# Optimization experiments

Measured on AMD Instinct MI355X. Metric: run time of the kernel, lower is better.

## Reference

```python
import jax, jax.numpy as jnp
import numpy as np

B, T, E, H, W = 2, 1024, 1024, 8, 31
D = 2 * W + 1  # head dim must equal 2*window_size+1 for the rel-pos broadcast


def _ln(x, w, b):
    mu = jnp.mean(x, axis=-1, keepdims=True)
    var = jnp.mean(jnp.square(x - mu), axis=-1, keepdims=True)
    return (x - mu) * jax.lax.rsqrt(var + 1e-5) * w + b


def setup_inputs() -> dict:
    key = jax.random.key(0)
    k = jax.random.split(key, 8)
    s = 0.02
    return {
        "x": jax.random.normal(k[0], (B, T, E // 2), jnp.float32),
        "ln1_w": jnp.ones(E, jnp.float32), "ln1_b": jnp.zeros(E, jnp.float32),
        "qkv_w": jax.random.normal(k[1], (3 * H * D, E), jnp.float32) * s,
        "qkv_b": jnp.zeros(3 * H * D, jnp.float32),
        "rel_pos": jax.random.normal(k[2], (D, D), jnp.float32) * s,
        "proj_w": jax.random.normal(k[3], (E, H * D), jnp.float32) * s,
        "proj_b": jnp.zeros(E, jnp.float32),
        "ln2_w": jnp.ones(E, jnp.float32), "ln2_b": jnp.zeros(E, jnp.float32),
        "fc_w": jax.random.normal(k[4], (4 * E, E), jnp.float32) * s,
        "fc_b": jnp.zeros(4 * E, jnp.float32),
        "cproj_w": jax.random.normal(k[5], (E, 4 * E), jnp.float32) * s,
        "cproj_b": jnp.zeros(E, jnp.float32),
    }


def reference(x, ln1_w, ln1_b, qkv_w, qkv_b, rel_pos, proj_w, proj_b,
              ln2_w, ln2_b, fc_w, fc_b, cproj_w, cproj_b):
    # --- RotaryEmbedding: angle = x * inv_freq; out = cat(sin, cos) -> [B,T,E]
    dim = 2 * x.shape[-1]
    inv_freq = 1.0 / 10000.0 ** (jnp.arange(0, dim, 2, dtype=jnp.float32) / dim)
    ang = x * inv_freq
    xr = jnp.concatenate([jnp.sin(ang), jnp.cos(ang)], axis=-1)  # [B,T,E]

    # --- custom windowed attention on ln_1(xr)
    h = _ln(xr, ln1_w, ln1_b)
    qkv = h @ qkv_w.T + qkv_b                       # [B,T,3*H*D]
    q, k, v = jnp.split(qkv, 3, axis=-1)

    def heads(t):
        return t.reshape(B, T, H, D).transpose(0, 2, 1, 3)  # [B,H,T,D]

    q, k, v = heads(q), heads(k), heads(v)
    # per-token q-outer-k scores (einsum '...bd,...bv->...bdv'): [B,H,T,D,D]
    scores = jnp.einsum('bhtd,bhtv->bhtdv', q, k)
    # rel-pos bias: Embedding lookup at offsets -W..W (negative indices wrap)
    bias = rel_pos[jnp.arange(-W, W + 1) % D]       # [D, D] == [2W+1, d_model]
    attn = jax.nn.softmax(scores + bias, axis=-2)   # softmax over non-canonical axis
    out = jnp.einsum('bhtdv,bhtv->bhtd', attn, v)   # apply per-token attn matrix to v
    out = out.transpose(0, 2, 1, 3).reshape(B, T, H * D)
    xa = xr + out @ proj_w.T + proj_b               # residual

    # --- MLP
    h2 = _ln(xa, ln2_w, ln2_b)
    m = jax.nn.gelu(h2 @ fc_w.T + fc_b, approximate=False) @ cproj_w.T + cproj_b
    return xa + m
```

## Files before the change

kernel.cpp:

```cpp
#include <hip/hip_runtime.h>
#include <hip/hip_bf16.h>


typedef __bf16 bf16;
typedef bf16 bf16x8 __attribute__((ext_vector_type(8)));
typedef bf16 bf16x4 __attribute__((ext_vector_type(4)));
typedef bf16 bf16x2 __attribute__((ext_vector_type(2)));
typedef float f32x4 __attribute__((ext_vector_type(4)));

__global__ __launch_bounds__(256) void rotary_ln_kernel(
    const float* __restrict__ x, const float* __restrict__ w,
    const float* __restrict__ b, float* __restrict__ xr, bf16* __restrict__ Y)
{
    const int row = blockIdx.x;
    const int tid = threadIdx.x;
    float2 xv = *(const float2*)(x + (size_t)row * 512 + tid * 2);
    float i0 = exp2f(-(float)(2*tid)     * 0.025952563241307518f);
    float i1 = exp2f(-(float)(2*tid + 1) * 0.025952563241307518f);
    float a0 = xv.x * i0, a1 = xv.y * i1;
    float s0 = sinf(a0), s1 = sinf(a1);
    float c0 = cosf(a0), c1 = cosf(a1);
    *(float2*)(xr + (size_t)row * 1024 + tid*2)       = make_float2(s0, s1);
    *(float2*)(xr + (size_t)row * 1024 + 512 + tid*2) = make_float2(c0, c1);
    float s  = s0 + s1 + c0 + c1;
    float ss = s0*s0 + s1*s1 + c0*c0 + c1*c1;
    #pragma unroll
    for (int off = 32; off > 0; off >>= 1) {
        s  += __shfl_down(s, off);
        ss += __shfl_down(ss, off);
    }
    __shared__ float rs[4], rss[4];
    int wave = tid >> 6, lane = tid & 63;
    if (lane == 0) { rs[wave] = s; rss[wave] = ss; }
    __syncthreads();
    s  = rs[0] + rs[1] + rs[2] + rs[3];
    ss = rss[0] + rss[1] + rss[2] + rss[3];
    float mu   = s * (1.f / 1024.f);
    float var  = ss * (1.f / 1024.f) - mu * mu;
    float rstd = rsqrtf(var + 1e-5f);
    float2 w0 = *(const float2*)(w + tid*2);
    float2 b0 = *(const float2*)(b + tid*2);
    float2 w1 = *(const float2*)(w + 512 + tid*2);
    float2 b1 = *(const float2*)(b + 512 + tid*2);
    bf16x2 y0, y1;
    y0[0] = (bf16)((s0 - mu) * rstd * w0.x + b0.x);
    y0[1] = (bf16)((s1 - mu) * rstd * w0.y + b0.y);
    y1[0] = (bf16)((c0 - mu) * rstd * w1.x + b1.x);
    y1[1] = (bf16)((c1 - mu) * rstd * w1.y + b1.y);
    *(bf16x2*)(Y + (size_t)row * 1024 + tid*2)       = y0;
    *(bf16x2*)(Y + (size_t)row * 1024 + 512 + tid*2) = y1;
}

__global__ __launch_bounds__(256) void ln_bf16_kernel(
    const float* __restrict__ X, const float* __restrict__ w,
    const float* __restrict__ b, bf16* __restrict__ Y)
{
    int row = blockIdx.x;
    const float4* xp = (const float4*)(X + (size_t)row * 1024);
    float4 xv = xp[threadIdx.x];
    float s  = xv.x + xv.y + xv.z + xv.w;
    float ss = xv.x*xv.x + xv.y*xv.y + xv.z*xv.z + xv.w*xv.w;
    #pragma unroll
    for (int off = 32; off > 0; off >>= 1) {
        s  += __shfl_down(s, off);
        ss += __shfl_down(ss, off);
    }
    __shared__ float rs[4], rss[4];
    int wave = threadIdx.x >> 6, lane = threadIdx.x & 63;
    if (lane == 0) { rs[wave] = s; rss[wave] = ss; }
    __syncthreads();
    s  = rs[0] + rs[1] + rs[2] + rs[3];
    ss = rss[0] + rss[1] + rss[2] + rss[3];
    float mu  = s * (1.f / 1024.f);
    float var = ss * (1.f / 1024.f) - mu * mu;
    float rstd = rsqrtf(var + 1e-5f);
    float4 wv = ((const float4*)w)[threadIdx.x];
    float4 bv = ((const float4*)b)[threadIdx.x];
    bf16 y[4];
    y[0] = (bf16)((xv.x - mu) * rstd * wv.x + bv.x);
    y[1] = (bf16)((xv.y - mu) * rstd * wv.y + bv.y);
    y[2] = (bf16)((xv.z - mu) * rstd * wv.z + bv.z);
    y[3] = (bf16)((xv.w - mu) * rstd * wv.w + bv.w);
    *(uint2*)(Y + (size_t)row * 1024 + threadIdx.x * 4) = *(uint2*)y;
}

__device__ __forceinline__ void conv_chunk(
    const float* __restrict__ src, bf16* __restrict__ dst,
    int ci, int N, int K, int Kp)
{
    int kpc = Kp >> 3;
    int r  = ci / kpc;
    int kc = (ci - r * kpc) << 3;
    bf16x8 o;
    if (r < N && kc < K) {
        float4 f0 = *(const float4*)(src + (size_t)r * K + kc);
        float4 f1 = *(const float4*)(src + (size_t)r * K + kc + 4);
        o[0]=(bf16)f0.x; o[1]=(bf16)f0.y; o[2]=(bf16)f0.z; o[3]=(bf16)f0.w;
        o[4]=(bf16)f1.x; o[5]=(bf16)f1.y; o[6]=(bf16)f1.z; o[7]=(bf16)f1.w;
    } else {
        #pragma unroll
        for (int j = 0; j < 8; ++j) o[j] = (bf16)0.f;
    }
    *(bf16x8*)(dst + (size_t)r * Kp + kc) = o;
}

__global__ __launch_bounds__(256) void conv_all_kernel(
    const float* __restrict__ qkv_w, const float* __restrict__ proj_w,
    const float* __restrict__ fc_w,  const float* __restrict__ cproj_w,
    const float* __restrict__ qkv_b,
    bf16* __restrict__ wqkv, bf16* __restrict__ wproj,
    bf16* __restrict__ wfc,  bf16* __restrict__ wcproj,
    float* __restrict__ qkvb_p)
{
    if (blockIdx.x == 5120) {
        for (int i = threadIdx.x; i < 1536; i += 256)
            qkvb_p[i] = (i < 1512) ? qkv_b[i] : 0.f;
        return;
    }
    int idx = blockIdx.x * 256 + threadIdx.x;
    if      (idx < 196608)  conv_chunk(qkv_w,   wqkv,   idx,          1512, 1024, 1024);
    else if (idx < 262144)  conv_chunk(proj_w,  wproj,  idx - 196608, 1024,  504,  512);
    else if (idx < 786432)  conv_chunk(fc_w,    wfc,    idx - 262144, 4096, 1024, 1024);
    else                    conv_chunk(cproj_w, wcproj, idx - 786432, 1024, 4096, 4096);
}

template<int N> __device__ __forceinline__ void vmwait()
{
    if constexpr      (N==0) asm volatile("s_waitcnt vmcnt(0)" ::: "memory");
    else if constexpr (N==4) asm volatile("s_waitcnt vmcnt(4)" ::: "memory");
    else if constexpr (N==6) asm volatile("s_waitcnt vmcnt(6)" ::: "memory");
}
__device__ __forceinline__ void lgkmwait0()
{
    asm volatile("s_waitcnt lgkmcnt(0)" ::: "memory");
}
__device__ __forceinline__ void hw_barrier()
{
    asm volatile("s_barrier" ::: "memory");
}

__device__ __forceinline__ void gload16(const char* src, char* ldsdst)
{
    __builtin_amdgcn_global_load_lds(
        (const __attribute__((address_space(1))) void*)src,
        (__attribute__((address_space(3))) void*)ldsdst, 16, 0, 0);
}

__device__ __forceinline__ float gelu_exact(float v)
{
    return 0.5f * v * (1.f + erff(v * 0.70710678118654752f));
}

template<int EPI>
__global__ __launch_bounds__(512, 2) void gemm8_kernel(
    const bf16* __restrict__ A, const bf16* __restrict__ Wt,
    const float* __restrict__ bias, bf16* __restrict__ Cb,
    int N, int Kp, int ksplit)
{
    __shared__ __align__(16) char lds[131072];

    const int tid  = threadIdx.x;
    const int w    = tid >> 6;
    const int lane = tid & 63;
    const int wm   = w >> 2;
    const int wn   = w & 3;
    const int rl   = lane & 15;
    const int lh   = lane >> 4;

    const int gx = gridDim.x, gy = gridDim.y;
    const int nwg = gx * gy * gridDim.z;
    const int chunk = nwg >> 3;
    int id = (blockIdx.z * gy + blockIdx.y) * gx + blockIdx.x;
    int sw = (id & 7) * chunk + (id >> 3);
    const int bx = sw % gx;
    const int t2 = sw / gx;
    const int by = t2 % gy;
    const int bz = t2 / gy;

    const int row0 = by * 128;
    const int col0 = bx * 256;
    const size_t strideBy = (size_t)Kp * 2;
    const size_t kz = (size_t)bz * ksplit * 2;
    const char* Abase = (const char*)A  + (size_t)row0 * strideBy + kz;
    const char* Wbase = (const char*)Wt + (size_t)col0 * strideBy + kz;

    size_t srcA[2], srcB[4];
    #pragma unroll
    for (int i = 0; i < 2; ++i) {
        int ls = i * 512 + tid;
        int r = ls >> 3, s = ls & 7;
        srcA[i] = (size_t)r * strideBy + (size_t)((s ^ (r & 7)) << 4);
    }
    #pragma unroll
    for (int i = 0; i < 4; ++i) {
        int ls = i * 512 + tid;
        int r = ls >> 3, s = ls & 7;
        srcB[i] = (size_t)r * strideBy + (size_t)((s ^ (r & 7)) << 4);
    }

    auto STAGE_A = [&](int buf, int kt) {
        const char* ab = Abase + (size_t)kt * 128;
        char* d = &lds[buf * 16384];
        #pragma unroll
        for (int i = 0; i < 2; ++i)
            gload16(ab + srcA[i], d + (i * 512 + tid) * 16);
    };
    auto STAGE_B = [&](int buf, int kt) {
        const char* wb = Wbase + (size_t)kt * 128;
        char* d = &lds[32768 + buf * 32768];
        #pragma unroll
        for (int i = 0; i < 4; ++i)
            gload16(wb + srcB[i], d + (i * 512 + tid) * 16);
    };

    f32x4 acc[4][4] = {};
    const int niter = ksplit >> 6;

    STAGE_A(0, 0);
    STAGE_B(0, 0);
    STAGE_B(1, 1);
    vmwait<4>();
    hw_barrier();

    int cb3 = 0, sb3 = 2;
    for (int kt = 0; kt < niter; ++kt) {
        if (kt + 1 < niter) STAGE_A((kt + 1) & 1, kt + 1);
        if (kt + 2 < niter) STAGE_B(sb3, kt + 2);

        const char* pA = &lds[(kt & 1) * 16384];
        const char* pB = &lds[32768 + cb3 * 32768];
        bf16x8 af[4][2], bq[4][2];
        #pragma unroll
        for (int mi = 0; mi < 4; ++mi) {
            int ar = wm * 64 + mi * 16 + rl;
            #pragma unroll
            for (int ks = 0; ks < 2; ++ks)
                af[mi][ks] = *(const bf16x8*)
                    (pA + ar * 128 + (((ks * 4 + lh) ^ (ar & 7)) << 4));
        }
        #pragma unroll
        for (int nj = 0; nj < 4; ++nj) {
            int br = wn * 64 + nj * 16 + rl;
            #pragma unroll
            for (int ks = 0; ks < 2; ++ks)
                bq[nj][ks] = *(const bf16x8*)
                    (pB + br * 128 + (((ks * 4 + lh) ^ (br & 7)) << 4));
        }
        __builtin_amdgcn_s_setprio(1);
        #pragma unroll
        for (int ks = 0; ks < 2; ++ks)
            #pragma unroll
            for (int mi = 0; mi < 4; ++mi)
                #pragma unroll
                for (int nj = 0; nj < 4; ++nj)
                    acc[mi][nj] = __builtin_amdgcn_mfma_f32_16x16x32_bf16(
                        af[mi][ks], bq[nj][ks], acc[mi][nj], 0, 0, 0);
        __builtin_amdgcn_s_setprio(0);

        if (kt + 1 < niter) {
            lgkmwait0();
            if (kt + 2 < niter) vmwait<4>();
            else                vmwait<0>();
            hw_barrier();
        }
        cb3 = (cb3 == 2) ? 0 : cb3 + 1;
        sb3 = (sb3 == 2) ? 0 : sb3 + 1;
    }

    const int rq = lh * 4;
    bf16* Cbz = Cb;
    if (EPI == 3) Cbz += (size_t)bz * 2048 * N;
    #pragma unroll
    for (int mi = 0; mi < 4; ++mi) {
        #pragma unroll
        for (int rj = 0; rj < 4; ++rj) {
            int row = row0 + wm * 64 + mi * 16 + rq + rj;
            #pragma unroll
            for (int nj = 0; nj < 4; ++nj) {
                int col = col0 + wn * 64 + nj * 16 + rl;
                float c = acc[mi][nj][rj];
                size_t off = (size_t)row * N + col;
                if (EPI == 1) Cbz[off] = (bf16)gelu_exact(c + bias[col]);
                else          Cbz[off] = (bf16)c;
            }
        }
    }
}

template<int EPI>
__global__ __launch_bounds__(256, 4) void gemm6_kernel(
    const bf16* __restrict__ A, const bf16* __restrict__ Wt,
    const float* __restrict__ bias,
    float* Cf, bf16* Cb, int N, int Kp, int ksplit)
{
    __shared__ __align__(16) char lds[2][12288];

    const int tid  = threadIdx.x;
    const int w    = tid >> 6;
    const int lane = tid & 63;

    const int gx = gridDim.x, gy = gridDim.y;
    const int nwg = gx * gy * gridDim.z;
    const int chunk = nwg >> 3;
    int id = (blockIdx.z * gy + blockIdx.y) * gx + blockIdx.x;
    int sw = (id & 7) * chunk + (id >> 3);
    const int bx = sw % gx;
    const int t2 = sw / gx;
    const int by = t2 % gy;
    const int bz = t2 / gy;

    const int row0 = by * 64;
    const int col0 = bx * 128;
    const int wr = (w >> 1) * 32;
    const int wc = (w & 1) * 64;
    const int rl = lane & 15;
    const int kb16 = (lane >> 4) * 16;

    const size_t strideBy = (size_t)Kp * 2;
    const size_t kz = (size_t)bz * ksplit * 2;
    const char* Abase = (const char*)A  + (size_t)row0 * strideBy + kz;
    const char* Wbase = (const char*)Wt + (size_t)col0 * strideBy + kz;

    const size_t srcA0 = (size_t)(tid >> 2) * strideBy + (tid & 3) * 16;
    size_t srcB[2];
    #pragma unroll
    for (int i = 0; i < 2; ++i) {
        int o = (i * 256 + tid) * 16;
        srcB[i] = (size_t)(o >> 6) * strideBy + (o & 63);
    }

    f32x4 acc[2][4] = {};

    auto STAGE = [&](int buf, int kt) {
        const char* ab = Abase + (size_t)kt * 64;
        const char* wb = Wbase + (size_t)kt * 64;
        gload16(ab + srcA0, &lds[buf][0] + tid * 16);
        #pragma unroll
        for (int i = 0; i < 2; ++i)
            gload16(wb + srcB[i], &lds[buf][4096] + (i * 256 + tid) * 16);
    };

    const int niter = ksplit >> 5;
    STAGE(0, 0);
    __syncthreads();
    for (int kt = 0; kt < niter; ++kt) {
        if (kt + 1 < niter)
            STAGE((kt + 1) & 1, kt + 1);
        const char* base = lds[kt & 1];
        bf16x8 af[2], bfr[4];
        #pragma unroll
        for (int mi = 0; mi < 2; ++mi)
            af[mi] = *(const bf16x8*)(base + ((wr + mi*16 + rl) << 6) + kb16);
        #pragma unroll
        for (int nj = 0; nj < 4; ++nj)
            bfr[nj] = *(const bf16x8*)(base + 4096 + ((wc + nj*16 + rl) << 6) + kb16);
        __builtin_amdgcn_s_setprio(1);
        #pragma unroll
        for (int mi = 0; mi < 2; ++mi)
            #pragma unroll
            for (int nj = 0; nj < 4; ++nj)
                acc[mi][nj] = __builtin_amdgcn_mfma_f32_16x16x32_bf16(
                    af[mi], bfr[nj], acc[mi][nj], 0, 0, 0);
        __builtin_amdgcn_s_setprio(0);
        __syncthreads();
    }

    const int rq = (lane >> 4) * 4;
    bf16* Cbz = Cb;
    if (EPI == 3) Cbz += (size_t)bz * 2048 * N;
    #pragma unroll
    for (int mi = 0; mi < 2; ++mi) {
        #pragma unroll
        for (int rj = 0; rj < 4; ++rj) {
            int row = row0 + wr + mi*16 + rq + rj;
            #pragma unroll
            for (int nj = 0; nj < 4; ++nj) {
                int col = col0 + wc + nj*16 + rl;
                float c = acc[mi][nj][rj];
                if (EPI != 3) c += bias[col];
                size_t off = (size_t)row * N + col;
                if (EPI == 0)      Cb[off]  = (bf16)c;
                else               Cbz[off] = (bf16)c;
            }
        }
    }
}

template<int P>
__global__ __launch_bounds__(256) void reduce_kernel(
    const bf16* __restrict__ parts, const float* __restrict__ bias,
    const float* R, float* out)
{
    int row = blockIdx.x;
    int c = threadIdx.x * 4;
    size_t off = (size_t)row * 1024 + c;
    float4 bv = *(const float4*)(bias + c);
    float4 o = *(const float4*)(R + off);
    o.x += bv.x; o.y += bv.y; o.z += bv.z; o.w += bv.w;
    #pragma unroll
    for (int p = 0; p < P; ++p) {
        bf16x4 v = *(const bf16x4*)(parts + (size_t)p * 2048 * 1024 + off);
        o.x += (float)v[0]; o.y += (float)v[1];
        o.z += (float)v[2]; o.w += (float)v[3];
    }
    *(float4*)(out + off) = o;
}

__global__ __launch_bounds__(256) void attn_kernel(
    const bf16* __restrict__ qkv, const float* __restrict__ rel_pos,
    bf16* __restrict__ outp)
{
    __shared__ float sbias[64*65];
    __shared__ float kmw[4][3][64];
    for (int i = threadIdx.x; i < 63*63; i += 256) {
        int d = i / 63, v = i - d*63;
        sbias[d*65 + v] = rel_pos[((d + 32) % 63) * 63 + v];
    }
    __syncthreads();
    const int wave = threadIdx.x >> 6;
    const int lane = threadIdx.x & 63;
    const int tk  = blockIdx.x * 4 + wave;
    const int row = tk >> 3;
    const int h   = tk & 7;
    const bf16* base = qkv + (size_t)row * 1536 + h * 63;
    float q_own = 0.f, k_own = 0.f, v_own = 0.f;
    if (lane < 63) {
        q_own = (float)base[lane];
        k_own = (float)base[504 + lane];
        v_own = (float)base[1008 + lane];
    }
    float m = -1e30f;
    for (int d = 0; d < 63; ++d) {
        float qd = __shfl(q_own, d);
        m = fmaxf(m, fmaf(qd, k_own, sbias[d*65 + lane]));
    }
    float Z = 0.f;
    for (int d = 0; d < 63; ++d) {
        float qd = __shfl(q_own, d);
        Z += __expf(fmaf(qd, k_own, sbias[d*65 + lane]) - m);
    }
    kmw[wave][0][lane] = k_own;
    kmw[wave][1][lane] = m;
    kmw[wave][2][lane] = v_own / Z;
    float acc = 0.f;
    for (int v = 0; v < 63; ++v) {
        float s = fmaf(q_own, kmw[wave][0][v], sbias[lane*65 + v]) - kmw[wave][1][v];
        acc += __expf(s) * kmw[wave][2][v];
    }
    if (lane < 63)
        outp[(size_t)row * 512 + h*63 + lane] = (bf16)acc;
    if (h == 7 && lane == 63) {
        #pragma unroll
        for (int j = 0; j < 8; ++j)
            outp[(size_t)row * 512 + 504 + j] = (bf16)0.f;
    }
}

extern "C" void kernel_launch(void* const* d_in, const int* in_sizes, int n_in,
                              void* d_out, int out_size, void* d_ws, size_t ws_size,
                              hipStream_t stream)
{
    const float* x       = (const float*)d_in[0];
    const float* ln1_w   = (const float*)d_in[1];
    const float* ln1_b   = (const float*)d_in[2];
    const float* qkv_w   = (const float*)d_in[3];
    const float* qkv_b   = (const float*)d_in[4];
    const float* rel_pos = (const float*)d_in[5];
    const float* proj_w  = (const float*)d_in[6];
    const float* proj_b  = (const float*)d_in[7];
    const float* ln2_w   = (const float*)d_in[8];
    const float* ln2_b   = (const float*)d_in[9];
    const float* fc_w    = (const float*)d_in[10];
    const float* fc_b    = (const float*)d_in[11];
    const float* cproj_w = (const float*)d_in[12];
    const float* cproj_b = (const float*)d_in[13];
    float* out = (float*)d_out;

    char* p = (char*)d_ws;
    float* xr      = (float*)p;            p += (size_t)2048*1024*4;
    bf16*  h_bf    = (bf16*)p;             p += (size_t)2048*1024*2;
    bf16*  wqkv    = (bf16*)p;             p += (size_t)1536*1024*2;
    bf16*  wproj   = (bf16*)p;             p += (size_t)1024*512*2;
    bf16*  wfc     = (bf16*)p;             p += (size_t)4096*1024*2;
    bf16*  wcproj  = (bf16*)p;             p += (size_t)1024*4096*2;
    float* qkvb_p  = (float*)p;            p += 8192;
    bf16*  attn_bf = (bf16*)p;             p += (size_t)2048*512*2;
    bf16*  qkvb    = (bf16*)p;
    bf16*  fc_act  = (bf16*)p;
    bf16*  proj_part = qkvb;
    bf16*  cp_part = (bf16*)d_ws;

    conv_all_kernel<<<5121, 256, 0, stream>>>(qkv_w, proj_w, fc_w, cproj_w, qkv_b,
                                              wqkv, wproj, wfc, wcproj, qkvb_p);
    rotary_ln_kernel<<<2048, 256, 0, stream>>>(x, ln1_w, ln1_b, xr, h_bf);
    gemm6_kernel<0><<<dim3(12,32,1), 256, 0, stream>>>(h_bf, wqkv, qkvb_p,
                                                       nullptr, qkvb, 1536, 1024, 1024);
    attn_kernel<<<4096, 256, 0, stream>>>(qkvb, rel_pos, attn_bf);
    gemm6_kernel<3><<<dim3(8,32,2), 256, 0, stream>>>(attn_bf, wproj, nullptr,
                                                      nullptr, proj_part, 1024, 512, 256);
    reduce_kernel<2><<<2048, 256, 0, stream>>>(proj_part, proj_b, xr, out);
    ln_bf16_kernel<<<2048, 256, 0, stream>>>(out, ln2_w, ln2_b, h_bf);
    gemm8_kernel<1><<<dim3(16,16,1), 512, 0, stream>>>(h_bf, wfc, fc_b,
                                                       fc_act, 4096, 1024, 1024);
    gemm8_kernel<3><<<dim3(4,16,4), 512, 0, stream>>>(fc_act, wcproj, nullptr,
                                                      cp_part, 1024, 4096, 1024);
    reduce_kernel<4><<<2048, 256, 0, stream>>>(cp_part, cproj_b, out, out);
}
```

Measured before the change: 145.0 us.

## Restructure MLP GEMM main loop into interleaved four-phase LDS/MFMA pipeline

Replaces the MLP GEMM kernel's K loop with a new schedule. A uses a 3-deep LDS ring and B a 2-deep ring split into two column halves. Each K step now runs four MFMA sub-phases, with each phase's LDS fragment reads and the next global-to-LDS prefetches placed between barriers. The aim is to overlap LDS reads and global loads with matrix-core work and cut LDS footprint, at the cost of more barriers per iteration and tighter cross-wave sync.

Measured after the change: 144.5 us. About the same (-0.4%).

```diff
diff --git a/kernel.cpp b/kernel.cpp
--- a/kernel.cpp
+++ b/kernel.cpp
@@ -127,7 +127,6 @@
 template<int N> __device__ __forceinline__ void vmwait()
 {
     if constexpr      (N==0) asm volatile("s_waitcnt vmcnt(0)" ::: "memory");
-    else if constexpr (N==4) asm volatile("s_waitcnt vmcnt(4)" ::: "memory");
     else if constexpr (N==6) asm volatile("s_waitcnt vmcnt(6)" ::: "memory");
 }
 __device__ __forceinline__ void lgkmwait0()
@@ -138,26 +137,24 @@
 {
     asm volatile("s_barrier" ::: "memory");
 }
-
 __device__ __forceinline__ void gload16(const char* src, char* ldsdst)
 {
     __builtin_amdgcn_global_load_lds(
         (const __attribute__((address_space(1))) void*)src,
         (__attribute__((address_space(3))) void*)ldsdst, 16, 0, 0);
 }
-
 __device__ __forceinline__ float gelu_exact(float v)
 {
     return 0.5f * v * (1.f + erff(v * 0.70710678118654752f));
 }
 
 template<int EPI>
-__global__ __launch_bounds__(512, 2) void gemm8_kernel(
+__global__ __launch_bounds__(512, 2) void gemm8p_kernel(
     const bf16* __restrict__ A, const bf16* __restrict__ Wt,
     const float* __restrict__ bias, bf16* __restrict__ Cb,
     int N, int Kp, int ksplit)
 {
-    __shared__ __align__(16) char lds[131072];
+    __shared__ __align__(16) char lds[114688];
 
     const int tid  = threadIdx.x;
     const int w    = tid >> 6;
@@ -184,87 +181,124 @@
     const char* Abase = (const char*)A  + (size_t)row0 * strideBy + kz;
     const char* Wbase = (const char*)Wt + (size_t)col0 * strideBy + kz;
 
-    size_t srcA[2], srcB[4];
+    size_t aoff[2], boff[4];
     #pragma unroll
     for (int i = 0; i < 2; ++i) {
         int ls = i * 512 + tid;
         int r = ls >> 3, s = ls & 7;
-        srcA[i] = (size_t)r * strideBy + (size_t)((s ^ (r & 7)) << 4);
+        aoff[i] = (size_t)r * strideBy + (size_t)((s ^ (r & 7)) << 4);
     }
     #pragma unroll
     for (int i = 0; i < 4; ++i) {
         int ls = i * 512 + tid;
         int r = ls >> 3, s = ls & 7;
-        srcB[i] = (size_t)r * strideBy + (size_t)((s ^ (r & 7)) << 4);
-    }
-
-    auto STAGE_A = [&](int buf, int kt) {
-        const char* ab = Abase + (size_t)kt * 128;
-        char* d = &lds[buf * 16384];
+        boff[i] = (size_t)r * strideBy + (size_t)((s ^ (r & 7)) << 4);
+    }
+
+    auto STAGE_A = [&](int t) {
+        const char* g = Abase + (size_t)t * 128;
+        char* d = &lds[(t % 3) * 16384];
         #pragma unroll
         for (int i = 0; i < 2; ++i)
-            gload16(ab + srcA[i], d + (i * 512 + tid) * 16);
+            gload16(g + aoff[i], d + (i * 512 + tid) * 16);
     };
-    auto STAGE_B = [&](int buf, int kt) {
-        const char* wb = Wbase + (size_t)kt * 128;
-        char* d = &lds[32768 + buf * 32768];
-        #pragma unroll
-        for (int i = 0; i < 4; ++i)
-            gload16(wb + srcB[i], d + (i * 512 + tid) * 16);
+    auto STAGE_B = [&](int t) {
+        const char* g = Wbase + (size_t)t * 128;
+        #pragma unroll
+        for (int i = 0; i < 4; ++i) {
+            char* d = &lds[49152 + (i >> 1) * 32768 + (t & 1) * 16384];
+            gload16(g + boff[i], d + ((i & 1) * 512 + tid) * 16);
+        }
     };
 
+    const int bhalf = wn >> 1;
+    const int brow  = (wn & 1) * 64;
+
     f32x4 acc[4][4] = {};
-    const int niter = ksplit >> 6;
-
-    STAGE_A(0, 0);
-    STAGE_B(0, 0);
-    STAGE_B(1, 1);
-    vmwait<4>();
-    hw_barrier();
-
-    int cb3 = 0, sb3 = 2;
-    for (int kt = 0; kt < niter; ++kt) {
-        if (kt + 1 < niter) STAGE_A((kt + 1) & 1, kt + 1);
-        if (kt + 2 < niter) STAGE_B(sb3, kt + 2);
-
-        const char* pA = &lds[(kt & 1) * 16384];
-        const char* pB = &lds[32768 + cb3 * 32768];
-        bf16x8 af[4][2], bq[4][2];
+    const int nt = ksplit >> 6;
+
+    STAGE_A(0); STAGE_B(0); STAGE_A(1); STAGE_B(1);
+
+    for (int t = 0; t < nt; ++t) {
+        if (t == nt - 1) vmwait<0>(); else vmwait<6>();
+        hw_barrier();
+        const char* pA = &lds[(t % 3) * 16384];
+        const char* pB = &lds[49152 + bhalf * 32768 + (t & 1) * 16384];
+
+        bf16x8 af0[4], af1[4], bq0[4], bq1[4];
         #pragma unroll
         for (int mi = 0; mi < 4; ++mi) {
             int ar = wm * 64 + mi * 16 + rl;
-            #pragma unroll
-            for (int ks = 0; ks < 2; ++ks)
-                af[mi][ks] = *(const bf16x8*)
-                    (pA + ar * 128 + (((ks * 4 + lh) ^ (ar & 7)) << 4));
-        }
-        #pragma unroll
-        for (int nj = 0; nj < 4; ++nj) {
-            int br = wn * 64 + nj * 16 + rl;
-            #pragma unroll
-            for (int ks = 0; ks < 2; ++ks)
-                bq[nj][ks] = *(const bf16x8*)
-                    (pB + br * 128 + (((ks * 4 + lh) ^ (br & 7)) << 4));
-        }
+            af0[mi] = *(const bf16x8*)(pA + ar * 128 + ((lh ^ (ar & 7)) << 4));
+        }
+        #pragma unroll
+        for (int nj = 0; nj < 2; ++nj) {
+            int br = brow + nj * 16 + rl;
+            bq0[nj] = *(const bf16x8*)(pB + br * 128 + ((lh ^ (br & 7)) << 4));
+        }
+        if (t + 2 < nt) STAGE_A(t + 2);
+        lgkmwait0();
+        hw_barrier();
         __builtin_amdgcn_s_setprio(1);
         #pragma unroll
-        for (int ks = 0; ks < 2; ++ks)
-            #pragma unroll
-            for (int mi = 0; mi < 4; ++mi)
-                #pragma unroll
-                for (int nj = 0; nj < 4; ++nj)
-                    acc[mi][nj] = __builtin_amdgcn_mfma_f32_16x16x32_bf16(
-                        af[mi][ks], bq[nj][ks], acc[mi][nj], 0, 0, 0);
+        for (int mi = 0; mi < 4; ++mi)
+            #pragma unroll
+            for (int nj = 0; nj < 2; ++nj)
+                acc[mi][nj] = __builtin_amdgcn_mfma_f32_16x16x32_bf16(
+                    af0[mi], bq0[nj], acc[mi][nj], 0, 0, 0);
         __builtin_amdgcn_s_setprio(0);
 
-        if (kt + 1 < niter) {
-            lgkmwait0();
-            if (kt + 2 < niter) vmwait<4>();
-            else                vmwait<0>();
-            hw_barrier();
-        }
-        cb3 = (cb3 == 2) ? 0 : cb3 + 1;
-        sb3 = (sb3 == 2) ? 0 : sb3 + 1;
+        #pragma unroll
+        for (int nj = 2; nj < 4; ++nj) {
+            int br = brow + nj * 16 + rl;
+            bq0[nj] = *(const bf16x8*)(pB + br * 128 + ((lh ^ (br & 7)) << 4));
+        }
+        #pragma unroll
+        for (int nj = 0; nj < 2; ++nj) {
+            int br = brow + nj * 16 + rl;
+            bq1[nj] = *(const bf16x8*)(pB + br * 128 + (((4 + lh) ^ (br & 7)) << 4));
+        }
+        lgkmwait0();
+        hw_barrier();
+        __builtin_amdgcn_s_setprio(1);
+        #pragma unroll
+        for (int mi = 0; mi < 4; ++mi)
+            #pragma unroll
+            for (int nj = 2; nj < 4; ++nj)
+                acc[mi][nj] = __builtin_amdgcn_mfma_f32_16x16x32_bf16(
+                    af0[mi], bq0[nj], acc[mi][nj], 0, 0, 0);
+        __builtin_amdgcn_s_setprio(0);
+
+        #pragma unroll
+        for (int mi = 0; mi < 4; ++mi) {
+            int ar = wm * 64 + mi * 16 + rl;
+            af1[mi] = *(const bf16x8*)(pA + ar * 128 + (((4 + lh) ^ (ar & 7)) << 4));
+        }
+        #pragma unroll
+        for (int nj = 2; nj < 4; ++nj) {
+            int br = brow + nj * 16 + rl;
+            bq1[nj] = *(const bf16x8*)(pB + br * 128 + (((4 + lh) ^ (br & 7)) << 4));
+        }
+        lgkmwait0();
+        hw_barrier();
+        __builtin_amdgcn_s_setprio(1);
+        #pragma unroll
+        for (int mi = 0; mi < 4; ++mi)
+            #pragma unroll
+            for (int nj = 0; nj < 2; ++nj)
+                acc[mi][nj] = __builtin_amdgcn_mfma_f32_16x16x32_bf16(
+                    af1[mi], bq1[nj], acc[mi][nj], 0, 0, 0);
+        __builtin_amdgcn_s_setprio(0);
+
+        if (t + 2 < nt) STAGE_B(t + 2);
+        __builtin_amdgcn_s_setprio(1);
+        #pragma unroll
+        for (int mi = 0; mi < 4; ++mi)
+            #pragma unroll
+            for (int nj = 2; nj < 4; ++nj)
+                acc[mi][nj] = __builtin_amdgcn_mfma_f32_16x16x32_bf16(
+                    af1[mi], bq1[nj], acc[mi][nj], 0, 0, 0);
+        __builtin_amdgcn_s_setprio(0);
     }
 
     const int rq = lh * 4;
@@ -500,9 +534,9 @@
                                                       nullptr, proj_part, 1024, 512, 256);
     reduce_kernel<2><<<2048, 256, 0, stream>>>(proj_part, proj_b, xr, out);
     ln_bf16_kernel<<<2048, 256, 0, stream>>>(out, ln2_w, ln2_b, h_bf);
-    gemm8_kernel<1><<<dim3(16,16,1), 512, 0, stream>>>(h_bf, wfc, fc_b,
-                                                       fc_act, 4096, 1024, 1024);
-    gemm8_kernel<3><<<dim3(4,16,4), 512, 0, stream>>>(fc_act, wcproj, nullptr,
-                                                      cp_part, 1024, 4096, 1024);
+    gemm8p_kernel<1><<<dim3(16,16,1), 512, 0, stream>>>(h_bf, wfc, fc_b,
+                                                        fc_act, 4096, 1024, 1024);
+    gemm8p_kernel<3><<<dim3(4,16,4), 512, 0, stream>>>(fc_act, wcproj, nullptr,
+                                                       cp_part, 1024, 4096, 1024);
     reduce_kernel<4><<<2048, 256, 0, stream>>>(cp_part, cproj_b, out, out);
 }
```
